# Optimization experiments

Measured on AMD Instinct MI355X. Metric: run time of the kernel, lower is better.

The kernel has to match this reference:

```python
import jax, jax.numpy as jnp
import numpy as np

B, LONG, SHORT, D, NH, HD = 512, 1000, 50, 64, 4, 16
NUM_ITEMS, TOPK = 100000, 50
NBUCKETS, HASHL, HASHD = 1024, 4, 16  # NOTE: 4 hash layers of D//4 so concat matches item_dim (source default 3 is a shape bug)


def lin(x, w, b):
    return x @ w.T + b


def ln(x, g, b):
    m = x.mean(-1, keepdims=True)
    v = ((x - m) ** 2).mean(-1, keepdims=True)
    return (x - m) / jnp.sqrt(v + 1e-5) * g + b


def setup_inputs() -> dict:
    key = jax.random.key(0)
    ks = jax.random.split(key, 24)
    rn = lambda i, s: jax.random.normal(ks[i], s, jnp.float32) * 0.02
    emb = rn(0, (NUM_ITEMS + 1, D)).at[0].set(0.0)  # padding_idx=0 row zeroed
    return dict(
        user_features=jax.random.normal(ks[1], (B, D), jnp.float32),
        target_item_id=jax.random.randint(ks[2], (B,), 0, NUM_ITEMS + 1),
        short_hist_ids=jax.random.randint(ks[3], (B, SHORT), 0, NUM_ITEMS + 1),
        long_hist_ids=jax.random.randint(ks[4], (B, LONG), 0, NUM_ITEMS + 1),
        item_emb=emb,
        tproj_w=rn(5, (D, D)), tproj_b=jnp.zeros((D,), jnp.float32),
        attn_w1=rn(6, (64, 3 * D)), attn_b1=jnp.zeros((64,), jnp.float32),
        attn_w2=rn(7, (1, 64)), attn_b2=jnp.zeros((1,), jnp.float32),
        hash_emb=rn(8, (HASHL, NBUCKETS, HASHD)),
        sdim_w=rn(9, (D, D)), sdim_b=jnp.zeros((D,), jnp.float32),
        tf_qkv_w=rn(10, (2, 3 * D, D)), tf_qkv_b=jnp.zeros((2, 3 * D), jnp.float32),
        tf_out_w=rn(11, (2, D, D)), tf_out_b=jnp.zeros((2, D), jnp.float32),
        tf_ln1_g=jnp.ones((2, D), jnp.float32), tf_ln1_b=jnp.zeros((2, D), jnp.float32),
        tf_ff1_w=rn(12, (2, 2 * D, D)), tf_ff1_b=jnp.zeros((2, 2 * D), jnp.float32),
        tf_ff2_w=rn(13, (2, D, 2 * D)), tf_ff2_b=jnp.zeros((2, D), jnp.float32),
        tf_ln2_g=jnp.ones((2, D), jnp.float32), tf_ln2_b=jnp.zeros((2, D), jnp.float32),
        fus_w1=rn(14, (256, 4 * D)), fus_b1=jnp.zeros((256,), jnp.float32),
        fus_w2=rn(15, (128, 256)), fus_b2=jnp.zeros((128,), jnp.float32),
        fus_w3=rn(16, (1, 128)), fus_b3=jnp.zeros((1,), jnp.float32),
    )


def sim_forward(user_features, item_emb, tproj_w, tproj_b, attn_w1, attn_b1,
                attn_w2, attn_b2, hash_emb, sdim_w, sdim_b, tf_qkv_w, tf_qkv_b,
                tf_out_w, tf_out_b, tf_ln1_g, tf_ln1_b, tf_ff1_w, tf_ff1_b,
                tf_ff2_w, tf_ff2_b, tf_ln2_g, tf_ln2_b, fus_w1, fus_b1, fus_w2,
                fus_b2, fus_w3, fus_b3, target_item_id, short_hist_ids, long_hist_ids):
    # target projection
    target_emb = lin(item_emb[target_item_id], tproj_w, tproj_b)         # [B,D]
    # ---- hard search over long history ----
    long_emb = item_emb[long_hist_ids]                                    # [B,L,D]
    t = jnp.broadcast_to(target_emb[:, None, :], long_emb.shape)
    cc = jnp.concatenate([t, long_emb, long_emb * t], axis=-1)            # [B,L,3D]
    scores = lin(jax.nn.relu(lin(cc, attn_w1, attn_b1)), attn_w2, attn_b2)[..., 0]
    attn = jax.nn.softmax(scores, axis=-1)                                # [B,L]
    top_w, top_i = jax.lax.top_k(attn, TOPK)
    top_w = jax.nn.softmax(top_w, axis=-1)
    top_e = jnp.take_along_axis(long_emb, top_i[..., None], axis=1)       # [B,K,D]
    hard_repr = (top_w[..., None] * top_e).sum(axis=1)                    # [B,D]
    # ---- SDIM soft search ----
    bucket = long_hist_ids % NBUCKETS
    h = hash_emb[:, bucket].mean(axis=2)                                  # [HL,B,HD]
    hash_repr = jnp.moveaxis(h, 0, 1).reshape(h.shape[1], HASHL * HASHD)  # [B,D]
    soft_repr = lin(hash_repr + long_emb.mean(axis=1), sdim_w, sdim_b)    # [B,D]
    # ---- BST transformer over short history (post-norm, relu, dropout=eval) ----
    x = item_emb[short_hist_ids]                                          # [B,S,D]
    for l in range(2):
        qkv = lin(x, tf_qkv_w[l], tf_qkv_b[l])
        q, k, v = jnp.split(qkv, 3, axis=-1)
        q = q.reshape(B, SHORT, NH, HD); k = k.reshape(B, SHORT, NH, HD); v = v.reshape(B, SHORT, NH, HD)
        sc = jnp.einsum('bqhd,bkhd->bhqk', q, k) / np.sqrt(HD).astype(np.float32)
        a = jax.nn.softmax(sc, axis=-1)
        o = jnp.einsum('bhqk,bkhd->bqhd', a, v).reshape(B, SHORT, D)
        x = ln(x + lin(o, tf_out_w[l], tf_out_b[l]), tf_ln1_g[l], tf_ln1_b[l])
        f = lin(jax.nn.relu(lin(x, tf_ff1_w[l], tf_ff1_b[l])), tf_ff2_w[l], tf_ff2_b[l])
        x = ln(x + f, tf_ln2_g[l], tf_ln2_b[l])
    bst_repr = x.mean(axis=1)                                             # [B,D]
    # ---- fusion MLP ----
    combined = jnp.concatenate([user_features, hard_repr, soft_repr, bst_repr], axis=-1)
    hdn = jax.nn.relu(lin(combined, fus_w1, fus_b1))
    hdn = jax.nn.relu(lin(hdn, fus_w2, fus_b2))
    return lin(hdn, fus_w3, fus_b3)[..., 0]                               # [B]


def reference(user_features, target_item_id, short_hist_ids, long_hist_ids,
              item_emb, tproj_w, tproj_b, attn_w1, attn_b1, attn_w2, attn_b2,
              hash_emb, sdim_w, sdim_b, tf_qkv_w, tf_qkv_b, tf_out_w, tf_out_b,
              tf_ln1_g, tf_ln1_b, tf_ff1_w, tf_ff1_b, tf_ff2_w, tf_ff2_b,
              tf_ln2_g, tf_ln2_b, fus_w1, fus_b1, fus_w2, fus_b2, fus_w3, fus_b3):
    return sim_forward(user_features, item_emb, tproj_w, tproj_b, attn_w1, attn_b1,
                       attn_w2, attn_b2, hash_emb, sdim_w, sdim_b, tf_qkv_w, tf_qkv_b,
                       tf_out_w, tf_out_b, tf_ln1_g, tf_ln1_b, tf_ff1_w, tf_ff1_b,
                       tf_ff2_w, tf_ff2_b, tf_ln2_g, tf_ln2_b, fus_w1, fus_b1,
                       fus_w2, fus_b2, fus_w3, fus_b3, target_item_id,
                       short_hist_ids, long_hist_ids)
```

## Files before the change

kernel.cpp:

```cpp
#include <hip/hip_runtime.h>
#include <math.h>

#define NB 512
#define LONGN 1000
#define SHORTN 50
#define TOPKN 50
#define HALFN 500
#define NG 8
#define EROW 72
#define BROW 72
#define F1ROW 136

typedef __attribute__((ext_vector_type(8))) short bf16x8;
typedef __attribute__((ext_vector_type(4))) float f32x4;

__device__ __forceinline__ float dot4(float4 a, float4 b) {
  return a.x*b.x + a.y*b.y + a.z*b.z + a.w*b.w;
}

template<int N>
__device__ __forceinline__ float dotN(const float* w, const float* x) {
  const float4* w4 = (const float4*)w;
  const float4* x4 = (const float4*)x;
  float a0 = 0.f, a1 = 0.f, a2 = 0.f, a3 = 0.f;
  #pragma unroll
  for (int k = 0; k < N/4; k += 4) {
    a0 += dot4(w4[k],   x4[k]);
    a1 += dot4(w4[k+1], x4[k+1]);
    a2 += dot4(w4[k+2], x4[k+2]);
    a3 += dot4(w4[k+3], x4[k+3]);
  }
  return (a0 + a1) + (a2 + a3);
}

__device__ __forceinline__ float wave_sum(float v) {
  #pragma unroll
  for (int off = 32; off > 0; off >>= 1) v += __shfl_xor(v, off);
  return v;
}
__device__ __forceinline__ float wave_max(float v) {
  #pragma unroll
  for (int off = 32; off > 0; off >>= 1) v = fmaxf(v, __shfl_xor(v, off));
  return v;
}

__device__ __forceinline__ unsigned short f2bf(float x) {
  unsigned u = __float_as_uint(x);
  return (unsigned short)((u + 0x7fffu + ((u >> 16) & 1u)) >> 16);
}

__global__ __launch_bounds__(256, 3) void hard_scores_kernel(
    const int* __restrict__ target_item_id,
    const int* __restrict__ long_hist_ids,
    const float* __restrict__ item_emb,
    const float* __restrict__ tproj_w, const float* __restrict__ tproj_b,
    const float* __restrict__ attn_w1, const float* __restrict__ attn_b1,
    const float* __restrict__ attn_w2, const float* __restrict__ attn_b2,
    const float* __restrict__ hash_emb,
    float* __restrict__ scores_ws, float* __restrict__ partA,
    float* __restrict__ partH)
{
  __shared__ __align__(16) short Abf[64*EROW];
  __shared__ __align__(16) short Ebuf[2][64*EROW];
  __shared__ __align__(16) float tv[64];
  __shared__ __align__(16) float te[64];
  __shared__ __align__(16) float2 cw[64];
  __shared__ int idsL[HALFN];
  __shared__ __align__(16) float redE[4*64];

  const int bid = blockIdx.x;
  const int b = bid >> 1, half = bid & 1;
  const int base = half * HALFN;
  const int tid = threadIdx.x;
  const int wid = tid >> 6, lane = tid & 63;

  if (tid < 64) tv[tid] = item_emb[target_item_id[b]*64 + tid];
  for (int l = tid; l < HALFN; l += 256) idsL[l] = long_hist_ids[b*LONGN + base + l];
  __syncthreads();
  if (tid < 64) te[tid] = tproj_b[tid] + dotN<64>(tproj_w + tid*64, tv);
  __syncthreads();
  if (tid < 64) {
    float c = attn_b1[tid] + dotN<64>(attn_w1 + tid*192, te);
    cw[tid] = make_float2(c, attn_w2[tid]);
  }
  for (int idx = tid; idx < 4096; idx += 256) {
    int i = idx >> 6, j = idx & 63;
    Abf[i*EROW + j] = (short)f2bf(attn_w1[i*192 + 64 + j] + attn_w1[i*192 + 128 + j]*te[j]);
  }
  __syncthreads();

  bf16x8 a00,a01,a10,a11,a20,a21,a30,a31;
  {
    const short* ap = Abf + (lane & 15)*EROW + ((lane >> 4) << 3);
    a00 = *(const bf16x8*)(ap +  0*EROW);  a01 = *(const bf16x8*)(ap +  0*EROW + 32);
    a10 = *(const bf16x8*)(ap + 16*EROW);  a11 = *(const bf16x8*)(ap + 16*EROW + 32);
    a20 = *(const bf16x8*)(ap + 32*EROW);  a21 = *(const bf16x8*)(ap + 32*EROW + 32);
    a30 = *(const bf16x8*)(ap + 48*EROW);  a31 = *(const bf16x8*)(ap + 48*EROW + 32);
  }

  const float b2s = attn_b2[0];
  const int it_g = tid >> 2;
  const int dimg = (tid & 3) * 16;

  float4 sE0 = {0,0,0,0}, sE1 = {0,0,0,0}, sE2 = {0,0,0,0}, sE3 = {0,0,0,0};

  {
    const float4* ep = (const float4*)(item_emb + (size_t)idsL[it_g]*64 + dimg);
    float4 r0 = ep[0], r1 = ep[1], r2 = ep[2], r3 = ep[3];
    sE0.x+=r0.x; sE0.y+=r0.y; sE0.z+=r0.z; sE0.w+=r0.w;
    sE1.x+=r1.x; sE1.y+=r1.y; sE1.z+=r1.z; sE1.w+=r1.w;
    sE2.x+=r2.x; sE2.y+=r2.y; sE2.z+=r2.z; sE2.w+=r2.w;
    sE3.x+=r3.x; sE3.y+=r3.y; sE3.z+=r3.z; sE3.w+=r3.w;
    bf16x8 w0, w1;
    w0[0]=(short)f2bf(r0.x); w0[1]=(short)f2bf(r0.y); w0[2]=(short)f2bf(r0.z); w0[3]=(short)f2bf(r0.w);
    w0[4]=(short)f2bf(r1.x); w0[5]=(short)f2bf(r1.y); w0[6]=(short)f2bf(r1.z); w0[7]=(short)f2bf(r1.w);
    w1[0]=(short)f2bf(r2.x); w1[1]=(short)f2bf(r2.y); w1[2]=(short)f2bf(r2.z); w1[3]=(short)f2bf(r2.w);
    w1[4]=(short)f2bf(r3.x); w1[5]=(short)f2bf(r3.y); w1[6]=(short)f2bf(r3.z); w1[7]=(short)f2bf(r3.w);
    short* dst = &Ebuf[0][it_g*EROW + dimg];
    *(bf16x8*)dst = w0;  *(bf16x8*)(dst + 8) = w1;
  }
  __syncthreads();

  int buf = 0;
  for (int g = 0; g < NG; ++g) {
    float4 r0={0,0,0,0}, r1={0,0,0,0}, r2={0,0,0,0}, r3={0,0,0,0};
    const bool more = (g + 1 < NG);
    if (more) {
      const int gi = (g+1)*64 + it_g;
      if (gi < HALFN) {
        const float4* ep = (const float4*)(item_emb + (size_t)idsL[gi]*64 + dimg);
        r0 = ep[0]; r1 = ep[1]; r2 = ep[2]; r3 = ep[3];
      }
    }

    f32x4 acc0={0,0,0,0}, acc1={0,0,0,0}, acc2={0,0,0,0}, acc3={0,0,0,0};
    {
      const short* ep = &Ebuf[buf][(wid*16 + (lane & 15))*EROW + ((lane >> 4) << 3)];
      bf16x8 b0 = *(const bf16x8*)(ep);
      bf16x8 b1 = *(const bf16x8*)(ep + 32);
      acc0 = __builtin_amdgcn_mfma_f32_16x16x32_bf16(a00, b0, acc0, 0, 0, 0);
      acc0 = __builtin_amdgcn_mfma_f32_16x16x32_bf16(a01, b1, acc0, 0, 0, 0);
      acc1 = __builtin_amdgcn_mfma_f32_16x16x32_bf16(a10, b0, acc1, 0, 0, 0);
      acc1 = __builtin_amdgcn_mfma_f32_16x16x32_bf16(a11, b1, acc1, 0, 0, 0);
      acc2 = __builtin_amdgcn_mfma_f32_16x16x32_bf16(a20, b0, acc2, 0, 0, 0);
      acc2 = __builtin_amdgcn_mfma_f32_16x16x32_bf16(a21, b1, acc2, 0, 0, 0);
      acc3 = __builtin_amdgcn_mfma_f32_16x16x32_bf16(a30, b0, acc3, 0, 0, 0);
      acc3 = __builtin_amdgcn_mfma_f32_16x16x32_bf16(a31, b1, acc3, 0, 0, 0);
    }
    float p = 0.f;
    {
      const int rbase = (lane >> 4) << 2;
      #pragma unroll
      for (int r = 0; r < 4; ++r) {
        float2 c0 = cw[ 0 + rbase + r];
        float2 c1 = cw[16 + rbase + r];
        float2 c2 = cw[32 + rbase + r];
        float2 c3 = cw[48 + rbase + r];
        p += c0.y * fmaxf(acc0[r] + c0.x, 0.f);
        p += c1.y * fmaxf(acc1[r] + c1.x, 0.f);
        p += c2.y * fmaxf(acc2[r] + c2.x, 0.f);
        p += c3.y * fmaxf(acc3[r] + c3.x, 0.f);
      }
    }
    p += __shfl_xor(p, 16);
    p += __shfl_xor(p, 32);
    if (lane < 16) {
      const int gi = g*64 + wid*16 + lane;
      if (gi < HALFN) scores_ws[b*LONGN + base + gi] = b2s + p;
    }

    if (more) {
      sE0.x+=r0.x; sE0.y+=r0.y; sE0.z+=r0.z; sE0.w+=r0.w;
      sE1.x+=r1.x; sE1.y+=r1.y; sE1.z+=r1.z; sE1.w+=r1.w;
      sE2.x+=r2.x; sE2.y+=r2.y; sE2.z+=r2.z; sE2.w+=r2.w;
      sE3.x+=r3.x; sE3.y+=r3.y; sE3.z+=r3.z; sE3.w+=r3.w;
      bf16x8 w0, w1;
      w0[0]=(short)f2bf(r0.x); w0[1]=(short)f2bf(r0.y); w0[2]=(short)f2bf(r0.z); w0[3]=(short)f2bf(r0.w);
      w0[4]=(short)f2bf(r1.x); w0[5]=(short)f2bf(r1.y); w0[6]=(short)f2bf(r1.z); w0[7]=(short)f2bf(r1.w);
      w1[0]=(short)f2bf(r2.x); w1[1]=(short)f2bf(r2.y); w1[2]=(short)f2bf(r2.z); w1[3]=(short)f2bf(r2.w);
      w1[4]=(short)f2bf(r3.x); w1[5]=(short)f2bf(r3.y); w1[6]=(short)f2bf(r3.z); w1[7]=(short)f2bf(r3.w);
      short* dst = &Ebuf[buf ^ 1][it_g*EROW + dimg];
      *(bf16x8*)dst = w0;  *(bf16x8*)(dst + 8) = w1;
    }
    __syncthreads();
    buf ^= 1;
  }

  {
    float* red = (float*)&Ebuf[0][0];
    const int b17 = tid * 17;
    red[b17+ 0]=sE0.x; red[b17+ 1]=sE0.y; red[b17+ 2]=sE0.z; red[b17+ 3]=sE0.w;
    red[b17+ 4]=sE1.x; red[b17+ 5]=sE1.y; red[b17+ 6]=sE1.z; red[b17+ 7]=sE1.w;
    red[b17+ 8]=sE2.x; red[b17+ 9]=sE2.y; red[b17+10]=sE2.z; red[b17+11]=sE2.w;
    red[b17+12]=sE3.x; red[b17+13]=sE3.y; red[b17+14]=sE3.z; red[b17+15]=sE3.w;
    __syncthreads();
    if (tid < 64) {
      const int dg = tid >> 4, dw = tid & 15;
      float s = 0.f;
      for (int j = 0; j < 64; ++j) s += red[(j*4 + dg)*17 + dw];
      partA[bid*64 + tid] = s;
    }
  }

  {
    const int hl = lane >> 4, dd = lane & 15;
    const float* hb = hash_emb + hl*1024*16 + dd;
    float accH = 0.f;
    for (int l = wid; l < HALFN; l += 4)
      accH += hb[(idsL[l] & 1023)*16];
    redE[wid*64 + lane] = accH;
  }
  __syncthreads();
  if (wid == 0)
    partH[bid*64 + lane] = redE[lane] + redE[64+lane] + redE[128+lane] + redE[192+lane];
}

__global__ __launch_bounds__(256) void bst_prep_kernel(
    const float* __restrict__ qkv_w, const float* __restrict__ out_w,
    const float* __restrict__ ff1_w, const float* __restrict__ ff2_w,
    short* __restrict__ wF)
{
  const int t = blockIdx.x*256 + threadIdx.x;
  if (t >= 8192) return;
  const int fid = t >> 6, lane = t & 63;
  const int n16 = lane & 15, k8 = (lane >> 4) * 8;
  const float* src;
  if (fid < 48)      { int f=fid,    l=f/24, r=f%24, nt=r>>1, kc=r&1;
    src = qkv_w + l*12288 + (nt*16+n16)*64 + kc*32 + k8; }
  else if (fid < 64) { int f=fid-48, l=f>>3, r=f&7,  nt=r>>1, kc=r&1;
    src = out_w + l*4096 + (nt*16+n16)*64 + kc*32 + k8; }
  else if (fid < 96) { int f=fid-64, l=f>>4, r=f&15, nt=r>>1, kc=r&1;
    src = ff1_w + l*8192 + (nt*16+n16)*64 + kc*32 + k8; }
  else               { int f=fid-96, l=f>>4, r=f&15, nt=r>>2, kc=r&3;
    src = ff2_w + l*8192 + (nt*16+n16)*128 + kc*32 + k8; }
  short* dst = wF + fid*512 + lane*8;
  #pragma unroll
  for (int j = 0; j < 8; ++j) dst[j] = (short)f2bf(src[j]);
}

__global__ __launch_bounds__(512, 2) void bst_kernel(
    const int* __restrict__ short_ids, const float* __restrict__ item_emb,
    const short* __restrict__ wF,
    const float* __restrict__ qkv_b, const float* __restrict__ out_b,
    const float* __restrict__ ln1_g, const float* __restrict__ ln1_b,
    const float* __restrict__ ff1_b, const float* __restrict__ ff2_b,
    const float* __restrict__ ln2_g, const float* __restrict__ ln2_b,
    float* __restrict__ bst_out)
{
  __shared__ __align__(16) float xf[SHORTN*64];
  __shared__ __align__(16) short xbf[64*BROW];
  __shared__ __align__(16) float qf[SHORTN*68];
  __shared__ __align__(16) float arena[SHORTN*132];
  __shared__ __align__(16) short obf[64*BROW];

  short* f1bf = (short*)arena;

  const int b = blockIdx.x, tid = threadIdx.x;
  const int w8 = tid >> 6, lane = tid & 63;
  const int mh = w8 & 1, wg = w8 >> 1;
  const int n16 = lane & 15;
  const int kg8 = (lane >> 4) << 3;
  const int mrow = (lane >> 4) << 2;
  const int rb = 32*mh;

  for (int idx = tid; idx < SHORTN*64; idx += 512) {
    int s = idx >> 6, j = idx & 63;
    float v = item_emb[short_ids[b*SHORTN + s]*64 + j];
    xf[idx] = v;
    xbf[s*BROW + j] = (short)f2bf(v);
  }
  for (int idx = tid; idx < 14*BROW; idx += 512) {
    xbf[50*BROW + idx] = 0;
    obf[50*BROW + idx] = 0;
  }
  __syncthreads();

  for (int l = 0; l < 2; ++l) {
    {
      const short* ap = xbf + (rb + n16)*BROW + kg8;
      bf16x8 A00 = *(const bf16x8*)(ap);            bf16x8 A01 = *(const bf16x8*)(ap + 32);
      bf16x8 A10 = *(const bf16x8*)(ap + 16*BROW);  bf16x8 A11 = *(const bf16x8*)(ap + 16*BROW + 32);
      #pragma unroll
      for (int t = 0; t < 3; ++t) {
        const int nt = wg*3 + t;
        const short* bp = wF + (size_t)(l*24 + nt*2)*512 + lane*8;
        bf16x8 B0 = *(const bf16x8*)(bp);
        bf16x8 B1 = *(const bf16x8*)(bp + 512);
        f32x4 c0={0,0,0,0}, c1={0,0,0,0};
        c0 = __builtin_amdgcn_mfma_f32_16x16x32_bf16(A00, B0, c0, 0,0,0);
        c0 = __builtin_amdgcn_mfma_f32_16x16x32_bf16(A01, B1, c0, 0,0,0);
        c1 = __builtin_amdgcn_mfma_f32_16x16x32_bf16(A10, B0, c1, 0,0,0);
        c1 = __builtin_amdgcn_mfma_f32_16x16x32_bf16(A11, B1, c1, 0,0,0);
        const int c = nt*16 + n16;
        const float bias = qkv_b[l*192 + c];
        #pragma unroll
        for (int r = 0; r < 4; ++r) {
          const int r0 = rb + mrow + r;
          const int r1 = r0 + 16;
          float v0 = c0[r] + bias;
          float v1 = c1[r] + bias;
          if (c < 64) {
            qf[r0*68 + c] = v0;
            if (r1 < SHORTN) qf[r1*68 + c] = v1;
          } else {
            const int cc = c - 64;
            arena[r0*132 + cc] = v0;
            if (r1 < SHORTN) arena[r1*132 + cc] = v1;
          }
        }
      }
    }
    __syncthreads();

    if (tid < 4*SHORTN) {
      const int h = tid / SHORTN, s = tid - h*SHORTN;
      const float4* qp = (const float4*)(qf + s*68 + h*16);
      const float4 qA = qp[0], qB2 = qp[1], qC = qp[2], qD = qp[3];
      float m = -INFINITY, ss = 0.f;
      float4 oa0 = {0,0,0,0}, oa1 = {0,0,0,0}, oa2 = {0,0,0,0}, oa3 = {0,0,0,0};
      for (int t2 = 0; t2 < SHORTN; ++t2) {
        const float4* kp = (const float4*)(arena + t2*132 + h*16);
        float d = dot4(qA,kp[0]) + dot4(qB2,kp[1]) + dot4(qC,kp[2]) + dot4(qD,kp[3]);
        d *= 0.25f;
        float mn = fmaxf(m, d);
        float al = __expf(m - mn);
        float a  = __expf(d - mn);
        m = mn;
        ss = ss*al + a;
        const float4* vp = (const float4*)(arena + t2*132 + 64 + h*16);
        float4 v0 = vp[0], v1 = vp[1], v2 = vp[2], v3 = vp[3];
        oa0.x = oa0.x*al + a*v0.x; oa0.y = oa0.y*al + a*v0.y;
        oa0.z = oa0.z*al + a*v0.z; oa0.w = oa0.w*al + a*v0.w;
        oa1.x = oa1.x*al + a*v1.x; oa1.y = oa1.y*al + a*v1.y;
        oa1.z = oa1.z*al + a*v1.z; oa1.w = oa1.w*al + a*v1.w;
        oa2.x = oa2.x*al + a*v2.x; oa2.y = oa2.y*al + a*v2.y;
        oa2.z = oa2.z*al + a*v2.z; oa2.w = oa2.w*al + a*v2.w;
        oa3.x = oa3.x*al + a*v3.x; oa3.y = oa3.y*al + a*v3.y;
        oa3.z = oa3.z*al + a*v3.z; oa3.w = oa3.w*al + a*v3.w;
      }
      const float inv = 1.f/ss;
      bf16x8 w0, w1;
      w0[0]=(short)f2bf(oa0.x*inv); w0[1]=(short)f2bf(oa0.y*inv);
      w0[2]=(short)f2bf(oa0.z*inv); w0[3]=(short)f2bf(oa0.w*inv);
      w0[4]=(short)f2bf(oa1.x*inv); w0[5]=(short)f2bf(oa1.y*inv);
      w0[6]=(short)f2bf(oa1.z*inv); w0[7]=(short)f2bf(oa1.w*inv);
      w1[0]=(short)f2bf(oa2.x*inv); w1[1]=(short)f2bf(oa2.y*inv);
      w1[2]=(short)f2bf(oa2.z*inv); w1[3]=(short)f2bf(oa2.w*inv);
      w1[4]=(short)f2bf(oa3.x*inv); w1[5]=(short)f2bf(oa3.y*inv);
      w1[6]=(short)f2bf(oa3.z*inv); w1[7]=(short)f2bf(oa3.w*inv);
      short* op = obf + s*BROW + h*16;
      *(bf16x8*)op = w0;  *(bf16x8*)(op + 8) = w1;
    }
    __syncthreads();

    {
      const short* ap = obf + (rb + n16)*BROW + kg8;
      bf16x8 A00 = *(const bf16x8*)(ap);            bf16x8 A01 = *(const bf16x8*)(ap + 32);
      bf16x8 A10 = *(const bf16x8*)(ap + 16*BROW);  bf16x8 A11 = *(const bf16x8*)(ap + 16*BROW + 32);
      const int nt = wg;
      const short* bp = wF + (size_t)(48 + l*8 + nt*2)*512 + lane*8;
      bf16x8 B0 = *(const bf16x8*)(bp);
      bf16x8 B1 = *(const bf16x8*)(bp + 512);
      f32x4 c0={0,0,0,0}, c1={0,0,0,0};
      c0 = __builtin_amdgcn_mfma_f32_16x16x32_bf16(A00, B0, c0, 0,0,0);
      c0 = __builtin_amdgcn_mfma_f32_16x16x32_bf16(A01, B1, c0, 0,0,0);
      c1 = __builtin_amdgcn_mfma_f32_16x16x32_bf16(A10, B0, c1, 0,0,0);
      c1 = __builtin_amdgcn_mfma_f32_16x16x32_bf16(A11, B1, c1, 0,0,0);
      const int c = nt*16 + n16;
      const float bias = out_b[l*64 + c];
      #pragma unroll
      for (int r = 0; r < 4; ++r) {
        const int r0 = rb + mrow + r;
        const int r1 = r0 + 16;
        arena[r0*68 + c] = xf[r0*64 + c] + bias + c0[r];
        if (r1 < SHORTN) arena[r1*68 + c] = xf[r1*64 + c] + bias + c1[r];
      }
      for (int idx = tid; idx < 14*F1ROW; idx += 512) f1bf[50*F1ROW + idx] = 0;
    }
    __syncthreads();

    {
      const float g = ln1_g[l*64 + lane], bb = ln1_b[l*64 + lane];
      for (int s = w8; s < SHORTN; s += 8) {
        float y = arena[s*68 + lane];
        float mean = wave_sum(y) * (1.f/64.f);
        float dv = y - mean;
        float var = wave_sum(dv*dv) * (1.f/64.f);
        float r = dv / sqrtf(var + 1e-5f) * g + bb;
        xf[s*64 + lane] = r;
        xbf[s*BROW + lane] = (short)f2bf(r);
      }
    }
    __syncthreads();

    {
      const short* ap = xbf + (rb + n16)*BROW + kg8;
      bf16x8 A00 = *(const bf16x8*)(ap);            bf16x8 A01 = *(const bf16x8*)(ap + 32);
      bf16x8 A10 = *(const bf16x8*)(ap + 16*BROW);  bf16x8 A11 = *(const bf16x8*)(ap + 16*BROW + 32);
      #pragma unroll
      for (int t = 0; t < 2; ++t) {
        const int nt = wg*2 + t;
        const short* bp = wF + (size_t)(64 + l*16 + nt*2)*512 + lane*8;
        bf16x8 B0 = *(const bf16x8*)(bp);
        bf16x8 B1 = *(const bf16x8*)(bp + 512);
        f32x4 c0={0,0,0,0}, c1={0,0,0,0};
        c0 = __builtin_amdgcn_mfma_f32_16x16x32_bf16(A00, B0, c0, 0,0,0);
        c0 = __builtin_amdgcn_mfma_f32_16x16x32_bf16(A01, B1, c0, 0,0,0);
        c1 = __builtin_amdgcn_mfma_f32_16x16x32_bf16(A10, B0, c1, 0,0,0);
        c1 = __builtin_amdgcn_mfma_f32_16x16x32_bf16(A11, B1, c1, 0,0,0);
        const int c = nt*16 + n16;
        const float bias = ff1_b[l*128 + c];
        #pragma unroll
        for (int r = 0; r < 4; ++r) {
          const int r0 = rb + mrow + r;
          const int r1 = r0 + 16;
          f1bf[r0*F1ROW + c] = (short)f2bf(fmaxf(c0[r] + bias, 0.f));
          if (r1 < SHORTN) f1bf[r1*F1ROW + c] = (short)f2bf(fmaxf(c1[r] + bias, 0.f));
        }
      }
    }
    __syncthreads();

    {
      const int nt = wg;
      f32x4 c0={0,0,0,0}, c1={0,0,0,0};
      #pragma unroll
      for (int kc = 0; kc < 4; ++kc) {
        const short* ap = f1bf + (rb + n16)*F1ROW + kc*32 + kg8;
        bf16x8 A0 = *(const bf16x8*)(ap);
        bf16x8 A1 = *(const bf16x8*)(ap + 16*F1ROW);
        const short* bp = wF + (size_t)(96 + l*16 + nt*4 + kc)*512 + lane*8;
        bf16x8 B = *(const bf16x8*)(bp);
        c0 = __builtin_amdgcn_mfma_f32_16x16x32_bf16(A0, B, c0, 0,0,0);
        c1 = __builtin_amdgcn_mfma_f32_16x16x32_bf16(A1, B, c1, 0,0,0);
      }
      __syncthreads();
      const int c = nt*16 + n16;
      const float bias = ff2_b[l*64 + c];
      #pragma unroll
      for (int r = 0; r < 4; ++r) {
        const int r0 = rb + mrow + r;
        const int r1 = r0 + 16;
        arena[r0*68 + c] = xf[r0*64 + c] + bias + c0[r];
        if (r1 < SHORTN) arena[r1*68 + c] = xf[r1*64 + c] + bias + c1[r];
      }
    }
    __syncthreads();

    {
      const float g = ln2_g[l*64 + lane], bb = ln2_b[l*64 + lane];
      for (int s = w8; s < SHORTN; s += 8) {
        float y = arena[s*68 + lane];
        float mean = wave_sum(y) * (1.f/64.f);
        float dv = y - mean;
        float var = wave_sum(dv*dv) * (1.f/64.f);
        float r = dv / sqrtf(var + 1e-5f) * g + bb;
        xf[s*64 + lane] = r;
        xbf[s*BROW + lane] = (short)f2bf(r);
      }
    }
    __syncthreads();
  }

  float acc = 0.f;
  for (int s = w8; s < SHORTN; s += 8) acc += xf[s*64 + lane];
  qf[w8*64 + lane] = acc;
  __syncthreads();
  if (w8 == 0) {
    float t = qf[lane];
    #pragma unroll
    for (int w = 1; w < 8; ++w) t += qf[w*64 + lane];
    bst_out[b*64 + lane] = t * (1.f/50.f);
  }
}

__global__ __launch_bounds__(256) void hard_finish_fusion_kernel(
    const int* __restrict__ long_hist_ids,
    const float* __restrict__ item_emb,
    const float* __restrict__ sdim_w, const float* __restrict__ sdim_b,
    const float* __restrict__ scores_ws,
    const float* __restrict__ partA, const float* __restrict__ partH,
    const float* __restrict__ user, const float* __restrict__ bst,
    const float* __restrict__ w1, const float* __restrict__ b1,
    const float* __restrict__ w2, const float* __restrict__ b2,
    const float* __restrict__ w3, const float* __restrict__ b3,
    float* __restrict__ out)
{
  __shared__ __align__(16) float scores[LONGN];
  __shared__ int   idsL[LONGN];
  __shared__ __align__(16) unsigned long long kv[1024];
  __shared__ __align__(16) float redE[4*64];
  __shared__ __align__(16) float vecbuf[64];
  __shared__ float redV[4];
  __shared__ float selV[TOPKN];
  __shared__ int   selI[TOPKN];
  __shared__ __align__(16) float comb[256];
  __shared__ __align__(16) float h1[256];
  __shared__ __align__(16) float h2[128];

  const int b = blockIdx.x;
  const int tid = threadIdx.x;
  const int wid = tid >> 6, lane = tid & 63;

  for (int l = tid; l < LONGN; l += 256) {
    scores[l] = scores_ws[b*LONGN + l];
    idsL[l] = long_hist_ids[b*LONGN + l];
  }
  if (tid < 64)       comb[tid] = user[b*64 + tid];
  else if (tid >= 192) comb[tid] = bst[b*64 + tid - 192];
  __syncthreads();

  if (tid < 64)
    vecbuf[tid] = (partA[(2*b)*64 + tid] + partA[(2*b+1)*64 + tid]
                 + partH[(2*b)*64 + tid] + partH[(2*b+1)*64 + tid]) * (1.f/1000.f);
  __syncthreads();
  if (tid < 64)
    comb[128 + tid] = sdim_b[tid] + dotN<64>(sdim_w + tid*64, vecbuf);

  float mx = -INFINITY;
  for (int l = tid; l < LONGN; l += 256) mx = fmaxf(mx, scores[l]);
  mx = wave_max(mx);
  if (lane == 0) redV[wid] = mx;
  __syncthreads();
  mx = fmaxf(fmaxf(redV[0], redV[1]), fmaxf(redV[2], redV[3]));
  __syncthreads();
  float sm = 0.f;
  for (int l = tid; l < LONGN; l += 256) {
    float a = expf(scores[l] - mx);
    scores[l] = a;
    sm += a;
  }
  sm = wave_sum(sm);
  if (lane == 0) redV[wid] = sm;
  __syncthreads();
  {
    const float inv = 1.f / (redV[0] + redV[1] + redV[2] + redV[3]);
    for (int l = tid; l < LONGN; l += 256) scores[l] *= inv;
  }
  __syncthreads();

  for (int l = tid; l < 1024; l += 256) {
    if (l < LONGN) {
      unsigned vb = __float_as_uint(scores[l]);
      kv[l] = ((unsigned long long)(~vb) << 32) | (unsigned)l;
    } else {
      kv[l] = 0xFFFFFFFFFFFFFFFFull;
    }
  }
  __syncthreads();

  for (int k = 2; k <= 1024; k <<= 1) {
    for (int j = k >> 1; j > 0; j >>= 1) {
      #pragma unroll 2
      for (int p = tid; p < 512; p += 256) {
        const int i = ((p & ~(j-1)) << 1) | (p & (j-1));
        const int m = i + j;
        const bool up = ((i & k) == 0);
        unsigned long long a = kv[i], c = kv[m];
        if ((a > c) == up) { kv[i] = c; kv[m] = a; }
      }
      __syncthreads();
    }
  }

  if (tid < TOPKN) {
    unsigned long long key = kv[tid];
    selI[tid] = (int)(unsigned)(key & 0xFFFFFFFFu);
    selV[tid] = __uint_as_float(~(unsigned)(key >> 32));
  }
  __syncthreads();

  if (wid == 0) {
    float v = (lane < TOPKN) ? selV[lane] : -INFINITY;
    float m2 = wave_max(v);
    float e = (lane < TOPKN) ? expf(v - m2) : 0.f;
    float s2 = wave_sum(e);
    if (lane < TOPKN) selV[lane] = e / s2;
  }
  __syncthreads();

  float accR = 0.f;
  for (int r = wid; r < TOPKN; r += 4)
    accR += selV[r] * item_emb[idsL[selI[r]]*64 + lane];
  redE[wid*64 + lane] = accR;
  __syncthreads();
  if (wid == 0)
    comb[64 + lane] = redE[lane] + redE[64+lane] + redE[128+lane] + redE[192+lane];
  __syncthreads();

  h1[tid] = fmaxf(b1[tid] + dotN<256>(w1 + tid*256, comb), 0.f);
  __syncthreads();
  if (tid < 128) h2[tid] = fmaxf(b2[tid] + dotN<256>(w2 + tid*256, h1), 0.f);
  __syncthreads();
  if (tid < 64) {
    float p = w3[tid]*h2[tid] + w3[tid+64]*h2[tid+64];
    p = wave_sum(p);
    if (tid == 0) out[b] = p + b3[0];
  }
}

extern "C" void kernel_launch(void* const* d_in, const int* in_sizes, int n_in,
                              void* d_out, int out_size, void* d_ws, size_t ws_size,
                              hipStream_t stream) {
  const float* user_features  = (const float*)d_in[0];
  const int*   target_item_id = (const int*)  d_in[1];
  const int*   short_hist_ids = (const int*)  d_in[2];
  const int*   long_hist_ids  = (const int*)  d_in[3];
  const float* item_emb       = (const float*)d_in[4];
  const float* tproj_w  = (const float*)d_in[5];
  const float* tproj_b  = (const float*)d_in[6];
  const float* attn_w1  = (const float*)d_in[7];
  const float* attn_b1  = (const float*)d_in[8];
  const float* attn_w2  = (const float*)d_in[9];
  const float* attn_b2  = (const float*)d_in[10];
  const float* hash_emb = (const float*)d_in[11];
  const float* sdim_w   = (const float*)d_in[12];
  const float* sdim_b   = (const float*)d_in[13];
  const float* tf_qkv_w = (const float*)d_in[14];
  const float* tf_qkv_b = (const float*)d_in[15];
  const float* tf_out_w = (const float*)d_in[16];
  const float* tf_out_b = (const float*)d_in[17];
  const float* tf_ln1_g = (const float*)d_in[18];
  const float* tf_ln1_b = (const float*)d_in[19];
  const float* tf_ff1_w = (const float*)d_in[20];
  const float* tf_ff1_b = (const float*)d_in[21];
  const float* tf_ff2_w = (const float*)d_in[22];
  const float* tf_ff2_b = (const float*)d_in[23];
  const float* tf_ln2_g = (const float*)d_in[24];
  const float* tf_ln2_b = (const float*)d_in[25];
  const float* fus_w1   = (const float*)d_in[26];
  const float* fus_b1   = (const float*)d_in[27];
  const float* fus_w2   = (const float*)d_in[28];
  const float* fus_b2   = (const float*)d_in[29];
  const float* fus_w3   = (const float*)d_in[30];
  const float* fus_b3   = (const float*)d_in[31];

  float* ws = (float*)d_ws;
  float* hard = ws;
  float* soft = hard + NB*64;
  float* bst  = soft + NB*64;
  float* scores_ws = bst + NB*64;
  float* partA = scores_ws + NB*LONGN;
  float* partH = partA + NB*2*64;
  short* wF    = (short*)(partH + NB*2*64);

  bst_prep_kernel<<<32, 256, 0, stream>>>(tf_qkv_w, tf_out_w, tf_ff1_w, tf_ff2_w, wF);
  hard_scores_kernel<<<2*NB, 256, 0, stream>>>(target_item_id, long_hist_ids,
      item_emb, tproj_w, tproj_b, attn_w1, attn_b1, attn_w2, attn_b2,
      hash_emb, scores_ws, partA, partH);
  bst_kernel<<<NB, 512, 0, stream>>>(short_hist_ids, item_emb, wF,
      tf_qkv_b, tf_out_b, tf_ln1_g, tf_ln1_b, tf_ff1_b, tf_ff2_b,
      tf_ln2_g, tf_ln2_b, bst);
  hard_finish_fusion_kernel<<<NB, 256, 0, stream>>>(long_hist_ids, item_emb,
      sdim_w, sdim_b, scores_ws, partA, partH,
      user_features, bst, fus_w1, fus_b1, fus_w2, fus_b2, fus_w3, fus_b3,
      (float*)d_out);
}
```

Before: 165.2 us.

## Split BST attention keys across thread pairs and widen finish kernel to 512 threads

In the BST attention step, each (head, query) pair is now handled by two threads. Each thread covers half of the 50 keys using a plain exp without a running max, and the two partial sums are merged with a lane shuffle. The hard_finish_fusion kernel now runs 512 threads per block, so the softmax, bitonic sort and gather loops do one element per thread with 8-wave reductions. The hard_scores_kernel occupancy hint is also raised from 3 to 4. Dropping the max subtraction removes the rescaling cost but could overflow if attention logits get large, and the higher occupancy hint may cause register spills.

```diff
diff --git a/kernel.cpp b/kernel.cpp
--- a/kernel.cpp
+++ b/kernel.cpp
@@ -49,7 +49,7 @@
   return (unsigned short)((u + 0x7fffu + ((u >> 16) & 1u)) >> 16);
 }
 
-__global__ __launch_bounds__(256, 3) void hard_scores_kernel(
+__global__ __launch_bounds__(256, 4) void hard_scores_kernel(
     const int* __restrict__ target_item_id,
     const int* __restrict__ long_hist_ids,
     const float* __restrict__ item_emb,
@@ -312,44 +312,49 @@
     }
     __syncthreads();
 
-    if (tid < 4*SHORTN) {
-      const int h = tid / SHORTN, s = tid - h*SHORTN;
+    if (tid < 8*SHORTN) {
+      const int pair = tid >> 1, khalf = tid & 1;
+      const int h = pair / SHORTN, s = pair - h*SHORTN;
       const float4* qp = (const float4*)(qf + s*68 + h*16);
       const float4 qA = qp[0], qB2 = qp[1], qC = qp[2], qD = qp[3];
-      float m = -INFINITY, ss = 0.f;
+      float ss = 0.f;
       float4 oa0 = {0,0,0,0}, oa1 = {0,0,0,0}, oa2 = {0,0,0,0}, oa3 = {0,0,0,0};
-      for (int t2 = 0; t2 < SHORTN; ++t2) {
+      const int t0 = khalf*25;
+      for (int t2 = t0; t2 < t0 + 25; ++t2) {
         const float4* kp = (const float4*)(arena + t2*132 + h*16);
         float d = dot4(qA,kp[0]) + dot4(qB2,kp[1]) + dot4(qC,kp[2]) + dot4(qD,kp[3]);
-        d *= 0.25f;
-        float mn = fmaxf(m, d);
-        float al = __expf(m - mn);
-        float a  = __expf(d - mn);
-        m = mn;
-        ss = ss*al + a;
+        float p = __expf(d*0.25f);
+        ss += p;
         const float4* vp = (const float4*)(arena + t2*132 + 64 + h*16);
         float4 v0 = vp[0], v1 = vp[1], v2 = vp[2], v3 = vp[3];
-        oa0.x = oa0.x*al + a*v0.x; oa0.y = oa0.y*al + a*v0.y;
-        oa0.z = oa0.z*al + a*v0.z; oa0.w = oa0.w*al + a*v0.w;
-        oa1.x = oa1.x*al + a*v1.x; oa1.y = oa1.y*al + a*v1.y;
-        oa1.z = oa1.z*al + a*v1.z; oa1.w = oa1.w*al + a*v1.w;
-        oa2.x = oa2.x*al + a*v2.x; oa2.y = oa2.y*al + a*v2.y;
-        oa2.z = oa2.z*al + a*v2.z; oa2.w = oa2.w*al + a*v2.w;
-        oa3.x = oa3.x*al + a*v3.x; oa3.y = oa3.y*al + a*v3.y;
-        oa3.z = oa3.z*al + a*v3.z; oa3.w = oa3.w*al + a*v3.w;
-      }
-      const float inv = 1.f/ss;
-      bf16x8 w0, w1;
-      w0[0]=(short)f2bf(oa0.x*inv); w0[1]=(short)f2bf(oa0.y*inv);
-      w0[2]=(short)f2bf(oa0.z*inv); w0[3]=(short)f2bf(oa0.w*inv);
-      w0[4]=(short)f2bf(oa1.x*inv); w0[5]=(short)f2bf(oa1.y*inv);
-      w0[6]=(short)f2bf(oa1.z*inv); w0[7]=(short)f2bf(oa1.w*inv);
-      w1[0]=(short)f2bf(oa2.x*inv); w1[1]=(short)f2bf(oa2.y*inv);
-      w1[2]=(short)f2bf(oa2.z*inv); w1[3]=(short)f2bf(oa2.w*inv);
-      w1[4]=(short)f2bf(oa3.x*inv); w1[5]=(short)f2bf(oa3.y*inv);
-      w1[6]=(short)f2bf(oa3.z*inv); w1[7]=(short)f2bf(oa3.w*inv);
-      short* op = obf + s*BROW + h*16;
-      *(bf16x8*)op = w0;  *(bf16x8*)(op + 8) = w1;
+        oa0.x += p*v0.x; oa0.y += p*v0.y; oa0.z += p*v0.z; oa0.w += p*v0.w;
+        oa1.x += p*v1.x; oa1.y += p*v1.y; oa1.z += p*v1.z; oa1.w += p*v1.w;
+        oa2.x += p*v2.x; oa2.y += p*v2.y; oa2.z += p*v2.z; oa2.w += p*v2.w;
+        oa3.x += p*v3.x; oa3.y += p*v3.y; oa3.z += p*v3.z; oa3.w += p*v3.w;
+      }
+      ss    += __shfl_xor(ss, 1);
+      oa0.x += __shfl_xor(oa0.x, 1); oa0.y += __shfl_xor(oa0.y, 1);
+      oa0.z += __shfl_xor(oa0.z, 1); oa0.w += __shfl_xor(oa0.w, 1);
+      oa1.x += __shfl_xor(oa1.x, 1); oa1.y += __shfl_xor(oa1.y, 1);
+      oa1.z += __shfl_xor(oa1.z, 1); oa1.w += __shfl_xor(oa1.w, 1);
+      oa2.x += __shfl_xor(oa2.x, 1); oa2.y += __shfl_xor(oa2.y, 1);
+      oa2.z += __shfl_xor(oa2.z, 1); oa2.w += __shfl_xor(oa2.w, 1);
+      oa3.x += __shfl_xor(oa3.x, 1); oa3.y += __shfl_xor(oa3.y, 1);
+      oa3.z += __shfl_xor(oa3.z, 1); oa3.w += __shfl_xor(oa3.w, 1);
+      if (khalf == 0) {
+        const float inv = 1.f/ss;
+        bf16x8 w0, w1;
+        w0[0]=(short)f2bf(oa0.x*inv); w0[1]=(short)f2bf(oa0.y*inv);
+        w0[2]=(short)f2bf(oa0.z*inv); w0[3]=(short)f2bf(oa0.w*inv);
+        w0[4]=(short)f2bf(oa1.x*inv); w0[5]=(short)f2bf(oa1.y*inv);
+        w0[6]=(short)f2bf(oa1.z*inv); w0[7]=(short)f2bf(oa1.w*inv);
+        w1[0]=(short)f2bf(oa2.x*inv); w1[1]=(short)f2bf(oa2.y*inv);
+        w1[2]=(short)f2bf(oa2.z*inv); w1[3]=(short)f2bf(oa2.w*inv);
+        w1[4]=(short)f2bf(oa3.x*inv); w1[5]=(short)f2bf(oa3.y*inv);
+        w1[6]=(short)f2bf(oa3.z*inv); w1[7]=(short)f2bf(oa3.w*inv);
+        short* op = obf + s*BROW + h*16;
+        *(bf16x8*)op = w0;  *(bf16x8*)(op + 8) = w1;
+      }
     }
     __syncthreads();
 
@@ -474,7 +479,7 @@
   }
 }
 
-__global__ __launch_bounds__(256) void hard_finish_fusion_kernel(
+__global__ __launch_bounds__(512) void hard_finish_fusion_kernel(
     const int* __restrict__ long_hist_ids,
     const float* __restrict__ item_emb,
     const float* __restrict__ sdim_w, const float* __restrict__ sdim_b,
@@ -489,9 +494,9 @@
   __shared__ __align__(16) float scores[LONGN];
   __shared__ int   idsL[LONGN];
   __shared__ __align__(16) unsigned long long kv[1024];
-  __shared__ __align__(16) float redE[4*64];
+  __shared__ __align__(16) float redE[8*64];
   __shared__ __align__(16) float vecbuf[64];
-  __shared__ float redV[4];
+  __shared__ float redV[8];
   __shared__ float selV[TOPKN];
   __shared__ int   selI[TOPKN];
   __shared__ __align__(16) float comb[256];
@@ -502,12 +507,12 @@
   const int tid = threadIdx.x;
   const int wid = tid >> 6, lane = tid & 63;
 
-  for (int l = tid; l < LONGN; l += 256) {
+  for (int l = tid; l < LONGN; l += 512) {
     scores[l] = scores_ws[b*LONGN + l];
     idsL[l] = long_hist_ids[b*LONGN + l];
   }
-  if (tid < 64)       comb[tid] = user[b*64 + tid];
-  else if (tid >= 192) comb[tid] = bst[b*64 + tid - 192];
+  if (tid < 64)                          comb[tid] = user[b*64 + tid];
+  else if (tid >= 192 && tid < 256)      comb[tid] = bst[b*64 + tid - 192];
   __syncthreads();
 
   if (tid < 64)
@@ -518,14 +523,16 @@
     comb[128 + tid] = sdim_b[tid] + dotN<64>(sdim_w + tid*64, vecbuf);
 
   float mx = -INFINITY;
-  for (int l = tid; l < LONGN; l += 256) mx = fmaxf(mx, scores[l]);
+  for (int l = tid; l < LONGN; l += 512) mx = fmaxf(mx, scores[l]);
   mx = wave_max(mx);
   if (lane == 0) redV[wid] = mx;
   __syncthreads();
-  mx = fmaxf(fmaxf(redV[0], redV[1]), fmaxf(redV[2], redV[3]));
+  mx = redV[0];
+  #pragma unroll
+  for (int w = 1; w < 8; ++w) mx = fmaxf(mx, redV[w]);
   __syncthreads();
   float sm = 0.f;
-  for (int l = tid; l < LONGN; l += 256) {
+  for (int l = tid; l < LONGN; l += 512) {
     float a = expf(scores[l] - mx);
     scores[l] = a;
     sm += a;
@@ -534,12 +541,15 @@
   if (lane == 0) redV[wid] = sm;
   __syncthreads();
   {
-    const float inv = 1.f / (redV[0] + redV[1] + redV[2] + redV[3]);
-    for (int l = tid; l < LONGN; l += 256) scores[l] *= inv;
-  }
-  __syncthreads();
-
-  for (int l = tid; l < 1024; l += 256) {
+    float tot = redV[0];
+    #pragma unroll
+    for (int w = 1; w < 8; ++w) tot += redV[w];
+    const float inv = 1.f / tot;
+    for (int l = tid; l < LONGN; l += 512) scores[l] *= inv;
+  }
+  __syncthreads();
+
+  for (int l = tid; l < 1024; l += 512) {
     if (l < LONGN) {
       unsigned vb = __float_as_uint(scores[l]);
       kv[l] = ((unsigned long long)(~vb) << 32) | (unsigned)l;
@@ -551,8 +561,8 @@
 
   for (int k = 2; k <= 1024; k <<= 1) {
     for (int j = k >> 1; j > 0; j >>= 1) {
-      #pragma unroll 2
-      for (int p = tid; p < 512; p += 256) {
+      {
+        const int p = tid;
         const int i = ((p & ~(j-1)) << 1) | (p & (j-1));
         const int m = i + j;
         const bool up = ((i & k) == 0);
@@ -580,15 +590,19 @@
   __syncthreads();
 
   float accR = 0.f;
-  for (int r = wid; r < TOPKN; r += 4)
+  for (int r = wid; r < TOPKN; r += 8)
     accR += selV[r] * item_emb[idsL[selI[r]]*64 + lane];
   redE[wid*64 + lane] = accR;
   __syncthreads();
-  if (wid == 0)
-    comb[64 + lane] = redE[lane] + redE[64+lane] + redE[128+lane] + redE[192+lane];
-  __syncthreads();
-
-  h1[tid] = fmaxf(b1[tid] + dotN<256>(w1 + tid*256, comb), 0.f);
+  if (wid == 0) {
+    float t = redE[lane];
+    #pragma unroll
+    for (int w = 1; w < 8; ++w) t += redE[w*64 + lane];
+    comb[64 + lane] = t;
+  }
+  __syncthreads();
+
+  if (tid < 256) h1[tid] = fmaxf(b1[tid] + dotN<256>(w1 + tid*256, comb), 0.f);
   __syncthreads();
   if (tid < 128) h2[tid] = fmaxf(b2[tid] + dotN<256>(w2 + tid*256, h1), 0.f);
   __syncthreads();
@@ -651,7 +665,7 @@
   bst_kernel<<<NB, 512, 0, stream>>>(short_hist_ids, item_emb, wF,
       tf_qkv_b, tf_out_b, tf_ln1_g, tf_ln1_b, tf_ff1_b, tf_ff2_b,
       tf_ln2_g, tf_ln2_b, bst);
-  hard_finish_fusion_kernel<<<NB, 256, 0, stream>>>(long_hist_ids, item_emb,
+  hard_finish_fusion_kernel<<<NB, 512, 0, stream>>>(long_hist_ids, item_emb,
       sdim_w, sdim_b, scores_ws, partA, partH,
       user_features, bst, fus_w1, fus_b1, fus_w2, fus_b2, fus_w3, fus_b3,
       (float*)d_out);
```

Measured after the change: 141.5 us (median of 2 runs). -14.3%, faster.
